# Optimization experiments

Measured on AMD Instinct MI355X. Metric: run time of the kernel, lower is better.

The kernel has to match this reference:

```python
import jax, jax.numpy as jnp
import numpy as np

EMB = 1024
HEADS = 16
B, N = 2, 2048

def setup_inputs() -> dict:
    key = jax.random.key(0)
    ks = jax.random.split(key, 9)
    s = 1.0 / np.sqrt(EMB)
    return {
        "x": jax.random.normal(ks[0], (B, N, EMB), dtype=jnp.float32),
        "Wq": jax.random.normal(ks[1], (EMB, EMB), dtype=jnp.float32) * s,
        "bq": jax.random.normal(ks[2], (EMB,), dtype=jnp.float32) * 0.01,
        "Wk": jax.random.normal(ks[3], (EMB, EMB), dtype=jnp.float32) * s,
        "bk": jax.random.normal(ks[4], (EMB,), dtype=jnp.float32) * 0.01,
        "Wv": jax.random.normal(ks[5], (EMB, EMB), dtype=jnp.float32) * s,
        "bv": jax.random.normal(ks[6], (EMB,), dtype=jnp.float32) * 0.01,
        "Wo": jax.random.normal(ks[7], (EMB, EMB), dtype=jnp.float32) * s,
        "bo": jax.random.normal(ks[8], (EMB,), dtype=jnp.float32) * 0.01,
    }

def _split_heads(t):
    b, n, e = t.shape
    return t.reshape(b, n, HEADS, e // HEADS).transpose(0, 2, 1, 3)  # b h n d

def reference(x, Wq, bq, Wk, bk, Wv, bv, Wo, bo):
    q = _split_heads(x @ Wq + bq)
    k = _split_heads(x @ Wk + bk)
    v = _split_heads(x @ Wv + bv)
    # NOTE: original scales by sqrt(emb_size), not sqrt(head_dim)
    scaling = jnp.asarray(EMB, x.dtype) ** 0.5
    energy = jnp.einsum('bhqd,bhkd->bhqk', q, k)
    att = jax.nn.softmax(energy / scaling, axis=-1)
    out = jnp.einsum('bhqk,bhkd->bhqd', att, v)
    out = out.transpose(0, 2, 1, 3).reshape(x.shape[0], x.shape[1], EMB)
    return out @ Wo + bo
```

## Files before the change

kernel.cpp:

```cpp
#include <hip/hip_runtime.h>
#include <hip/hip_bf16.h>

typedef __bf16 bf16_t;
typedef bf16_t bf16x8 __attribute__((ext_vector_type(8)));
typedef float f32x4 __attribute__((ext_vector_type(4)));
typedef float f32x16 __attribute__((ext_vector_type(16)));

#define EMB 1024
#define HEADS 16
#define BATCH 2
#define SEQ 2048
#define HD 64
#define TOKENS (BATCH * SEQ)

__device__ __forceinline__ void gld16(bf16_t* lds_dst, const bf16_t* g_src) {
    __builtin_amdgcn_global_load_lds(
        (const __attribute__((address_space(1))) unsigned int*)g_src,
        (__attribute__((address_space(3))) unsigned int*)lds_dst, 16, 0, 0);
}

__device__ __forceinline__ unsigned cvt_pk_bf16(float lo, float hi) {
    unsigned r;
    asm("v_cvt_pk_bf16_f32 %0, %1, %2" : "=v"(r) : "v"(lo), "v"(hi));
    return r;
}

__device__ __forceinline__ float exp2_fast(float x) {
#if __has_builtin(__builtin_amdgcn_exp2f)
    return __builtin_amdgcn_exp2f(x);
#else
    return __expf(x * 0.69314718056f);
#endif
}

#define WAITV(N) asm volatile("s_waitcnt vmcnt(" #N ")" ::: "memory")
#define BAR() __builtin_amdgcn_s_barrier()

__global__ __launch_bounds__(256) void convert_x(const float* __restrict__ x,
                                                 bf16_t* __restrict__ xb) {
    size_t i = ((size_t)blockIdx.x * 256 + threadIdx.x) * 16;
    f32x4 v0 = *(const f32x4*)&x[i];
    f32x4 v1 = *(const f32x4*)&x[i + 4];
    f32x4 v2 = *(const f32x4*)&x[i + 8];
    f32x4 v3 = *(const f32x4*)&x[i + 12];
    bf16x8 o0, o1;
#pragma unroll
    for (int j = 0; j < 4; ++j) {
        o0[j] = (bf16_t)v0[j]; o0[4 + j] = (bf16_t)v1[j];
        o1[j] = (bf16_t)v2[j]; o1[4 + j] = (bf16_t)v3[j];
    }
    *(bf16x8*)&xb[i] = o0;
    *(bf16x8*)&xb[i + 8] = o1;
}

__global__ __launch_bounds__(256) void prep_w(
    const float* __restrict__ W0, const float* __restrict__ W1,
    const float* __restrict__ W2, const float* __restrict__ W3,
    bf16_t* __restrict__ T0, bf16_t* __restrict__ T1,
    bf16_t* __restrict__ T2, bf16_t* __restrict__ T3) {
    __shared__ __align__(16) bf16_t T[64][72];
    int z = blockIdx.z;
    const float* src = (z == 0) ? W0 : (z == 1) ? W1 : (z == 2) ? W2 : W3;
    bf16_t* dst = (z == 0) ? T0 : (z == 1) ? T1 : (z == 2) ? T2 : T3;
    int k0 = blockIdx.y * 64, n0 = blockIdx.x * 64;
    int r = threadIdx.x >> 2, c4 = (threadIdx.x & 3) * 16;
    f32x4 v[4];
#pragma unroll
    for (int q = 0; q < 4; ++q)
        v[q] = *(const f32x4*)&src[(size_t)(k0 + r) * 1024 + n0 + c4 + q * 4];
#pragma unroll
    for (int j = 0; j < 16; ++j) T[c4 + j][r] = (bf16_t)v[j >> 2][j & 3];
    __syncthreads();
    bf16x8 o0 = *(const bf16x8*)&T[r][c4];
    bf16x8 o1 = *(const bf16x8*)&T[r][c4 + 8];
    *(bf16x8*)&dst[(size_t)(n0 + r) * 1024 + k0 + c4] = o0;
    *(bf16x8*)&dst[(size_t)(n0 + r) * 1024 + k0 + c4 + 8] = o1;
}

template <typename TO>
__global__ __launch_bounds__(512) void gemm256(
    const bf16_t* __restrict__ A, const bf16_t* __restrict__ W,
    const float* __restrict__ b0, const float* __restrict__ b1, const float* __restrict__ b2,
    TO* __restrict__ o0, TO* __restrict__ o1, TO* __restrict__ o2,
    int md0, int md1, int md2, float sc0, float sc1, float sc2,
    int MP, int CM, int CSH, int NP) {
    __shared__ __align__(16) bf16_t As[3][256 * 64];
    __shared__ __align__(16) bf16_t Bs[3][128 * 64];

    const int tid = threadIdx.x, w = tid >> 6, lane = tid & 63;
    const int quad = lane >> 4, c = lane & 15;
    const int wm = (w >> 1) * 64, wn = (w & 1) * 64;

    const int lin = blockIdx.x;
    const int xc = lin & 7, t = lin >> 3;
    const int mi = MP * (xc & CM) + (t % MP);
    const int ni = NP * (xc >> CSH) + (t / MP);
    const int m0 = mi * 256, n0 = ni * 128;

    const int z = n0 >> 10;
    const float* bias = (z == 0) ? b0 : (z == 1) ? b1 : b2;
    TO* out = (z == 0) ? o0 : (z == 1) ? o1 : o2;
    const int mode = (z == 0) ? md0 : (z == 1) ? md1 : md2;
    const float scale = (z == 0) ? sc0 : (z == 1) ? sc1 : sc2;
    const int nz = n0 & 1023;

    f32x4 acc[4][4];
#pragma unroll
    for (int i = 0; i < 4; ++i)
#pragma unroll
        for (int j = 0; j < 4; ++j) acc[i][j] = (f32x4){0.f, 0.f, 0.f, 0.f};

    const int r8 = lane >> 3, sg = lane & 7;
    const int g8 = (sg ^ r8) * 8;
    const bf16_t* Ag = A + (size_t)m0 * 1024;
    const bf16_t* Bg = W + (size_t)n0 * 1024;
    int gA[4], lA[4], gB[2], lB[2];
#pragma unroll
    for (int s = 0; s < 4; ++s) {
        lA[s] = (w * 32 + s * 8) * 64;
        gA[s] = (w * 32 + s * 8 + r8) * 1024 + g8;
    }
#pragma unroll
    for (int s = 0; s < 2; ++s) {
        lB[s] = (w * 16 + s * 8) * 64;
        gB[s] = (w * 16 + s * 8 + r8) * 1024 + g8;
    }

    const int so = (quad ^ (c & 7)) * 8;
    int rA[4], rB[4];
#pragma unroll
    for (int i = 0; i < 4; ++i) {
        rA[i] = (wm + i * 16 + c) * 64;
        rB[i] = (wn + i * 16 + c) * 64;
    }

#define STAGE(BUF, T)                                                          \
    {                                                                          \
        int kn = (T) * 64;                                                     \
        _Pragma("unroll")                                                      \
        for (int s = 0; s < 4; ++s) gld16(&As[BUF][lA[s]], &Ag[gA[s] + kn]);   \
        _Pragma("unroll")                                                      \
        for (int s = 0; s < 2; ++s) gld16(&Bs[BUF][lB[s]], &Bg[gB[s] + kn]);   \
    }

#define FRAGS(CUR)                                                             \
    {                                                                          \
        _Pragma("unroll")                                                      \
        for (int ks = 0; ks < 2; ++ks) {                                       \
            int sk = so ^ (ks << 5);                                           \
            bf16x8 af[4], bfv[4];                                              \
            _Pragma("unroll")                                                  \
            for (int i = 0; i < 4; ++i)                                        \
                af[i] = *(const bf16x8*)&As[CUR][rA[i] + sk];                  \
            _Pragma("unroll")                                                  \
            for (int i = 0; i < 4; ++i)                                        \
                bfv[i] = *(const bf16x8*)&Bs[CUR][rB[i] + sk];                 \
            __builtin_amdgcn_s_setprio(1);                                     \
            _Pragma("unroll")                                                  \
            for (int mt = 0; mt < 4; ++mt)                                     \
                _Pragma("unroll")                                              \
                for (int nt = 0; nt < 4; ++nt)                                 \
                    acc[mt][nt] = __builtin_amdgcn_mfma_f32_16x16x32_bf16(     \
                        af[mt], bfv[nt], acc[mt][nt], 0, 0, 0);                \
            __builtin_amdgcn_s_setprio(0);                                     \
        }                                                                      \
    }

#define GSTEP(T, CUR)                                                          \
    {                                                                          \
        WAITV(6);                                                              \
        BAR();                                                                 \
        STAGE(((CUR) + 2) % 3, (T) + 2)                                        \
        FRAGS(CUR)                                                             \
    }

    STAGE(0, 0)
    STAGE(1, 1)
    for (int T = 0; T < 12; T += 3) {
        GSTEP(T, 0)
        GSTEP(T + 1, 1)
        GSTEP(T + 2, 2)
    }
    GSTEP(12, 0)
    GSTEP(13, 1)
    WAITV(6); BAR(); FRAGS(2)
    WAITV(0); BAR(); FRAGS(0)
#undef GSTEP
#undef FRAGS
#undef STAGE

    typedef TO TOx4 __attribute__((ext_vector_type(4)));
#pragma unroll
    for (int nt = 0; nt < 4; ++nt) {
        int colz = nz + wn + nt * 16 + c;
        float bv = bias[colz];
#pragma unroll
        for (int mt = 0; mt < 4; ++mt) {
            if (mode == 2) {
                int row = m0 + wm + mt * 16 + quad * 4;
                int bb = row >> 11, n = row & 2047;
                int hh = colz >> 6, d = colz & 63;
                TOx4 pk;
#pragma unroll
                for (int r = 0; r < 4; ++r)
                    pk[r] = (TO)((acc[mt][nt][r] + bv) * scale);
                *(TOx4*)&out[((size_t)(bb * HEADS + hh) * HD + d) * SEQ + n] = pk;
            } else {
#pragma unroll
                for (int r = 0; r < 4; ++r) {
                    int row = m0 + wm + mt * 16 + quad * 4 + r;
                    float v = (acc[mt][nt][r] + bv) * scale;
                    size_t idx;
                    if (mode == 0) {
                        idx = (size_t)row * 1024 + colz;
                    } else {
                        int bb = row >> 11, n = row & 2047;
                        int hh = colz >> 6, d = colz & 63;
                        idx = ((size_t)(bb * HEADS + hh) * SEQ + n) * HD + d;
                    }
                    out[idx] = (TO)v;
                }
            }
        }
    }
}

__global__ __launch_bounds__(256) void attn_kernel(
    const bf16_t* __restrict__ Q, const bf16_t* __restrict__ K,
    const bf16_t* __restrict__ Vt, bf16_t* __restrict__ O) {
    __shared__ __align__(16) bf16_t Qs[128 * 64];
    __shared__ __align__(16) bf16_t Ks[3][64 * 64];
    __shared__ __align__(16) bf16_t Vs[3][64 * 64];

    const int tid = threadIdx.x, w = tid >> 6, lane = tid & 63;
    const int hi = lane >> 5, lq = lane & 31;

    const int lin = blockIdx.x + (blockIdx.y << 4);
    const int xcd = lin & 7, slot = lin >> 3;
    const int bh = xcd + ((slot >> 4) << 3);
    const int q0 = (slot & 15) << 7;
    const int b = bh >> 4, h = bh & 15;

    const int srow8 = lane >> 3, sch = lane & 7;

    const bf16_t* Qg = Q + ((size_t)bh * SEQ + q0) * HD;
    const bf16_t* Kg0 = K + (size_t)bh * SEQ * HD;
    const bf16_t* Vg0 = Vt + (size_t)bh * HD * SEQ;

    int sl[2], sgK[2], sgV[2];
#pragma unroll
    for (int s = 0; s < 2; ++s) {
        int rg = (w * 2 + s) * 8;
        int row = rg + srow8;
        int g = sch ^ (row & 7);
        sl[s] = rg * 64;
        sgK[s] = row * 64 + g * 8;
        sgV[s] = row * SEQ + g * 8;
    }
    int rd[4];
#pragma unroll
    for (int dc = 0; dc < 4; ++dc)
        rd[dc] = lq * 64 + (((dc * 2 + hi) ^ (lq & 7)) * 8);

#pragma unroll
    for (int s = 0; s < 4; ++s) {
        int rg = (w * 4 + s) * 8;
        int row = rg + srow8;
        int g = sch ^ (row & 7);
        gld16(&Qs[rg * 64], &Qg[(size_t)row * 64 + g * 8]);
    }
#pragma unroll
    for (int s = 0; s < 2; ++s) {
        gld16(&Ks[0][sl[s]], &Kg0[sgK[s]]);
        gld16(&Vs[0][sl[s]], &Vg0[sgV[s]]);
    }
#pragma unroll
    for (int s = 0; s < 2; ++s) {
        gld16(&Ks[1][sl[s]], &Kg0[64 * HD + sgK[s]]);
        gld16(&Vs[1][sl[s]], &Vg0[64 + sgV[s]]);
    }

    WAITV(8);
    BAR();
    bf16x8 qf[4];
#pragma unroll
    for (int dc = 0; dc < 4; ++dc)
        qf[dc] = *(const bf16x8*)&Qs[w * 2048 + rd[dc]];

    f32x16 Oacc0, Oacc1;
#pragma unroll
    for (int r = 0; r < 16; ++r) { Oacc0[r] = 0.f; Oacc1[r] = 0.f; }
    float lp = 0.f;

    const bf16_t* KgN = Kg0 + 2 * 64 * HD;
    const bf16_t* VgN = Vg0 + 2 * 64;

#define PACKFRAG(SS, c2, dstIdx)                                               \
        {                                                                      \
            unsigned pa = cvt_pk_bf16(SS[8 * (c2) + 0], SS[8 * (c2) + 1]);     \
            unsigned pb = cvt_pk_bf16(SS[8 * (c2) + 4], SS[8 * (c2) + 5]);     \
            unsigned pc = cvt_pk_bf16(SS[8 * (c2) + 2], SS[8 * (c2) + 3]);     \
            unsigned pd = cvt_pk_bf16(SS[8 * (c2) + 6], SS[8 * (c2) + 7]);     \
            asm volatile("v_permlane32_swap_b32 %0, %1" : "+v"(pa), "+v"(pb)); \
            asm volatile("v_permlane32_swap_b32 %0, %1" : "+v"(pc), "+v"(pd)); \
            union { unsigned u[4]; bf16x8 v; } pu;                             \
            pu.u[0] = pa; pu.u[1] = pc; pu.u[2] = pb; pu.u[3] = pd;            \
            pf[dstIdx] = pu.v;                                                 \
        }

#define ACORE(CUR)                                                             \
    {                                                                          \
        f32x16 St0, St1;                                                       \
        _Pragma("unroll")                                                      \
        for (int r = 0; r < 16; ++r) { St0[r] = 0.f; St1[r] = 0.f; }           \
        __builtin_amdgcn_s_setprio(1);                                         \
        _Pragma("unroll")                                                      \
        for (int dc = 0; dc < 4; ++dc) {                                       \
            bf16x8 k0 = *(const bf16x8*)&Ks[CUR][rd[dc]];                      \
            bf16x8 k1 = *(const bf16x8*)&Ks[CUR][rd[dc] + 2048];               \
            St0 = __builtin_amdgcn_mfma_f32_32x32x16_bf16(k0, qf[dc], St0, 0, 0, 0); \
            St1 = __builtin_amdgcn_mfma_f32_32x32x16_bf16(k1, qf[dc], St1, 0, 0, 0); \
        }                                                                      \
        __builtin_amdgcn_s_setprio(0);                                         \
        _Pragma("unroll")                                                      \
        for (int r = 0; r < 16; ++r) {                                         \
            St0[r] = exp2_fast(St0[r]); lp += St0[r];                          \
            St1[r] = exp2_fast(St1[r]); lp += St1[r];                          \
        }                                                                      \
        bf16x8 pf[4];                                                          \
        PACKFRAG(St0, 0, 0) PACKFRAG(St0, 1, 1)                                \
        PACKFRAG(St1, 0, 2) PACKFRAG(St1, 1, 3)                                \
        __builtin_amdgcn_s_setprio(1);                                         \
        _Pragma("unroll")                                                      \
        for (int f = 0; f < 4; ++f) {                                          \
            bf16x8 v0 = *(const bf16x8*)&Vs[CUR][rd[f]];                       \
            bf16x8 v1 = *(const bf16x8*)&Vs[CUR][rd[f] + 2048];                \
            Oacc0 = __builtin_amdgcn_mfma_f32_32x32x16_bf16(pf[f], v0, Oacc0, 0, 0, 0); \
            Oacc1 = __builtin_amdgcn_mfma_f32_32x32x16_bf16(pf[f], v1, Oacc1, 0, 0, 0); \
        }                                                                      \
        __builtin_amdgcn_s_setprio(0);                                         \
    }

#define ASTEP(CUR)                                                             \
    {                                                                          \
        WAITV(4);                                                              \
        BAR();                                                                 \
        _Pragma("unroll")                                                      \
        for (int s = 0; s < 2; ++s) {                                          \
            gld16(&Ks[((CUR) + 2) % 3][sl[s]], &KgN[sgK[s]]);                  \
            gld16(&Vs[((CUR) + 2) % 3][sl[s]], &VgN[sgV[s]]);                  \
        }                                                                      \
        KgN += 64 * HD; VgN += 64;                                             \
        ACORE(CUR)                                                             \
    }

    for (int t = 0; t < 30; t += 3) {
        ASTEP(0) ASTEP(1) ASTEP(2)
    }
    WAITV(4); BAR(); ACORE(0)
    WAITV(0); BAR(); ACORE(1)
#undef ASTEP
#undef ACORE
#undef PACKFRAG

    lp += __shfl_xor(lp, 32);
    float rl = 1.0f / lp;

#pragma unroll
    for (int r = 0; r < 16; ++r) {
        int q_loc = (r & 3) + 8 * (r >> 2) + 4 * hi;
        float rr = __shfl(rl, q_loc);
        int qrow = q0 + w * 32 + q_loc;
        size_t base = ((size_t)(b * SEQ + qrow)) * EMB + h * 64;
        O[base + lq] = (bf16_t)(Oacc0[r] * rr);
        O[base + 32 + lq] = (bf16_t)(Oacc1[r] * rr);
    }
}

extern "C" void kernel_launch(void* const* d_in, const int* in_sizes, int n_in,
                              void* d_out, int out_size, void* d_ws, size_t ws_size,
                              hipStream_t stream) {
    (void)in_sizes; (void)n_in; (void)out_size; (void)ws_size;
    const float* x  = (const float*)d_in[0];
    const float* Wq = (const float*)d_in[1];
    const float* bq = (const float*)d_in[2];
    const float* Wk = (const float*)d_in[3];
    const float* bk = (const float*)d_in[4];
    const float* Wv = (const float*)d_in[5];
    const float* bv = (const float*)d_in[6];
    const float* Wo = (const float*)d_in[7];
    const float* bo = (const float*)d_in[8];

    bf16_t* ws = (bf16_t*)d_ws;
    const size_t NELEM = (size_t)TOKENS * EMB;
    const size_t WELEM = (size_t)EMB * EMB;
    bf16_t* Qb  = ws;
    bf16_t* Kb  = ws + NELEM;
    bf16_t* Vtb = ws + 2 * NELEM;
    bf16_t* Ob  = ws + 3 * NELEM;
    bf16_t* xb  = ws + 4 * NELEM;
    bf16_t* Wt0 = ws + 5 * NELEM;
    bf16_t* Wt1 = Wt0 + WELEM;
    bf16_t* Wt2 = Wt0 + 2 * WELEM;
    bf16_t* Wt3 = Wt0 + 3 * WELEM;

    hipLaunchKernelGGL(convert_x, dim3(1024), dim3(256), 0, stream, x, xb);
    hipLaunchKernelGGL(prep_w, dim3(16, 16, 4), dim3(256), 0, stream,
                       Wq, Wk, Wv, Wo, Wt0, Wt1, Wt2, Wt3);
    hipLaunchKernelGGL((gemm256<bf16_t>), dim3(384), dim3(512), 0, stream,
                       xb, Wt0, bq, bk, bv, Qb, Kb, Vtb,
                       1, 1, 2, 0.0450842204f, 1.0f, 1.0f,
                       4, 3, 2, 12);
    hipLaunchKernelGGL(attn_kernel, dim3(16, 32), dim3(256), 0, stream, Qb, Kb, Vtb, Ob);
    hipLaunchKernelGGL((gemm256<float>), dim3(128), dim3(512), 0, stream,
                       Ob, Wt3, bo, bo, bo,
                       (float*)d_out, (float*)d_out, (float*)d_out,
                       0, 0, 0, 1.0f, 1.0f, 1.0f,
                       2, 7, 3, 8);
}
```

Before: 203.7 us.

## Merge prep kernels, load Q directly to registers, trim attention inner loop

Fuses the x conversion and weight transpose kernels into one launch, which removes a kernel launch and its tail. In attention, Q fragments are loaded straight from global memory into registers instead of going through LDS, which drops the Q shared buffer and the initial barrier. The first QK MFMA now uses a zero accumulator instead of explicitly zeroing the scores. The softmax row sum is split into paired vector accumulators to shorten the dependency chain. The direct Q loads are uncoalesced 16-byte reads, and the smaller LDS footprint may change occupancy.

```diff
diff --git a/kernel.cpp b/kernel.cpp
--- a/kernel.cpp
+++ b/kernel.cpp
@@ -4,6 +4,7 @@
 typedef __bf16 bf16_t;
 typedef bf16_t bf16x8 __attribute__((ext_vector_type(8)));
 typedef float f32x4 __attribute__((ext_vector_type(4)));
+typedef float f32x2 __attribute__((ext_vector_type(2)));
 typedef float f32x16 __attribute__((ext_vector_type(16)));
 
 #define EMB 1024
@@ -36,33 +37,34 @@
 #define WAITV(N) asm volatile("s_waitcnt vmcnt(" #N ")" ::: "memory")
 #define BAR() __builtin_amdgcn_s_barrier()
 
-__global__ __launch_bounds__(256) void convert_x(const float* __restrict__ x,
-                                                 bf16_t* __restrict__ xb) {
-    size_t i = ((size_t)blockIdx.x * 256 + threadIdx.x) * 16;
-    f32x4 v0 = *(const f32x4*)&x[i];
-    f32x4 v1 = *(const f32x4*)&x[i + 4];
-    f32x4 v2 = *(const f32x4*)&x[i + 8];
-    f32x4 v3 = *(const f32x4*)&x[i + 12];
-    bf16x8 o0, o1;
-#pragma unroll
-    for (int j = 0; j < 4; ++j) {
-        o0[j] = (bf16_t)v0[j]; o0[4 + j] = (bf16_t)v1[j];
-        o1[j] = (bf16_t)v2[j]; o1[4 + j] = (bf16_t)v3[j];
-    }
-    *(bf16x8*)&xb[i] = o0;
-    *(bf16x8*)&xb[i + 8] = o1;
-}
-
-__global__ __launch_bounds__(256) void prep_w(
+__global__ __launch_bounds__(256) void prep_all(
+    const float* __restrict__ x, bf16_t* __restrict__ xb,
     const float* __restrict__ W0, const float* __restrict__ W1,
     const float* __restrict__ W2, const float* __restrict__ W3,
     bf16_t* __restrict__ T0, bf16_t* __restrict__ T1,
     bf16_t* __restrict__ T2, bf16_t* __restrict__ T3) {
     __shared__ __align__(16) bf16_t T[64][72];
-    int z = blockIdx.z;
+    if (blockIdx.x < 1024) {
+        size_t i = ((size_t)blockIdx.x * 256 + threadIdx.x) * 16;
+        f32x4 v0 = *(const f32x4*)&x[i];
+        f32x4 v1 = *(const f32x4*)&x[i + 4];
+        f32x4 v2 = *(const f32x4*)&x[i + 8];
+        f32x4 v3 = *(const f32x4*)&x[i + 12];
+        bf16x8 o0, o1;
+#pragma unroll
+        for (int j = 0; j < 4; ++j) {
+            o0[j] = (bf16_t)v0[j]; o0[4 + j] = (bf16_t)v1[j];
+            o1[j] = (bf16_t)v2[j]; o1[4 + j] = (bf16_t)v3[j];
+        }
+        *(bf16x8*)&xb[i] = o0;
+        *(bf16x8*)&xb[i + 8] = o1;
+        return;
+    }
+    int t = blockIdx.x - 1024;
+    int z = t >> 8, rid = t & 255;
     const float* src = (z == 0) ? W0 : (z == 1) ? W1 : (z == 2) ? W2 : W3;
     bf16_t* dst = (z == 0) ? T0 : (z == 1) ? T1 : (z == 2) ? T2 : T3;
-    int k0 = blockIdx.y * 64, n0 = blockIdx.x * 64;
+    int k0 = (rid >> 4) * 64, n0 = (rid & 15) * 64;
     int r = threadIdx.x >> 2, c4 = (threadIdx.x & 3) * 16;
     f32x4 v[4];
 #pragma unroll
@@ -228,7 +230,6 @@
 __global__ __launch_bounds__(256) void attn_kernel(
     const bf16_t* __restrict__ Q, const bf16_t* __restrict__ K,
     const bf16_t* __restrict__ Vt, bf16_t* __restrict__ O) {
-    __shared__ __align__(16) bf16_t Qs[128 * 64];
     __shared__ __align__(16) bf16_t Ks[3][64 * 64];
     __shared__ __align__(16) bf16_t Vs[3][64 * 64];
 
@@ -243,7 +244,6 @@
 
     const int srow8 = lane >> 3, sch = lane & 7;
 
-    const bf16_t* Qg = Q + ((size_t)bh * SEQ + q0) * HD;
     const bf16_t* Kg0 = K + (size_t)bh * SEQ * HD;
     const bf16_t* Vg0 = Vt + (size_t)bh * HD * SEQ;
 
@@ -262,13 +262,14 @@
     for (int dc = 0; dc < 4; ++dc)
         rd[dc] = lq * 64 + (((dc * 2 + hi) ^ (lq & 7)) * 8);
 
-#pragma unroll
-    for (int s = 0; s < 4; ++s) {
-        int rg = (w * 4 + s) * 8;
-        int row = rg + srow8;
-        int g = sch ^ (row & 7);
-        gld16(&Qs[rg * 64], &Qg[(size_t)row * 64 + g * 8]);
-    }
+    bf16x8 qf[4];
+    {
+        const bf16_t* Qrow = Q + ((size_t)bh * SEQ + q0 + w * 32 + lq) * HD;
+#pragma unroll
+        for (int dc = 0; dc < 4; ++dc)
+            qf[dc] = *(const bf16x8*)&Qrow[(dc * 2 + hi) * 8];
+    }
+
 #pragma unroll
     for (int s = 0; s < 2; ++s) {
         gld16(&Ks[0][sl[s]], &Kg0[sgK[s]]);
@@ -280,17 +281,14 @@
         gld16(&Vs[1][sl[s]], &Vg0[64 + sgV[s]]);
     }
 
-    WAITV(8);
-    BAR();
-    bf16x8 qf[4];
-#pragma unroll
-    for (int dc = 0; dc < 4; ++dc)
-        qf[dc] = *(const bf16x8*)&Qs[w * 2048 + rd[dc]];
+    f32x16 Zf;
+#pragma unroll
+    for (int r = 0; r < 16; ++r) Zf[r] = 0.f;
 
     f32x16 Oacc0, Oacc1;
 #pragma unroll
     for (int r = 0; r < 16; ++r) { Oacc0[r] = 0.f; Oacc1[r] = 0.f; }
-    float lp = 0.f;
+    f32x2 lpA = (f32x2){0.f, 0.f}, lpB = (f32x2){0.f, 0.f};
 
     const bf16_t* KgN = Kg0 + 2 * 64 * HD;
     const bf16_t* VgN = Vg0 + 2 * 64;
@@ -311,11 +309,15 @@
 #define ACORE(CUR)                                                             \
     {                                                                          \
         f32x16 St0, St1;                                                       \
-        _Pragma("unroll")                                                      \
-        for (int r = 0; r < 16; ++r) { St0[r] = 0.f; St1[r] = 0.f; }           \
         __builtin_amdgcn_s_setprio(1);                                         \
-        _Pragma("unroll")                                                      \
-        for (int dc = 0; dc < 4; ++dc) {                                       \
+        {                                                                      \
+            bf16x8 k0 = *(const bf16x8*)&Ks[CUR][rd[0]];                       \
+            bf16x8 k1 = *(const bf16x8*)&Ks[CUR][rd[0] + 2048];                \
+            St0 = __builtin_amdgcn_mfma_f32_32x32x16_bf16(k0, qf[0], Zf, 0, 0, 0); \
+            St1 = __builtin_amdgcn_mfma_f32_32x32x16_bf16(k1, qf[0], Zf, 0, 0, 0); \
+        }                                                                      \
+        _Pragma("unroll")                                                      \
+        for (int dc = 1; dc < 4; ++dc) {                                       \
             bf16x8 k0 = *(const bf16x8*)&Ks[CUR][rd[dc]];                      \
             bf16x8 k1 = *(const bf16x8*)&Ks[CUR][rd[dc] + 2048];               \
             St0 = __builtin_amdgcn_mfma_f32_32x32x16_bf16(k0, qf[dc], St0, 0, 0, 0); \
@@ -323,9 +325,11 @@
         }                                                                      \
         __builtin_amdgcn_s_setprio(0);                                         \
         _Pragma("unroll")                                                      \
-        for (int r = 0; r < 16; ++r) {                                         \
-            St0[r] = exp2_fast(St0[r]); lp += St0[r];                          \
-            St1[r] = exp2_fast(St1[r]); lp += St1[r];                          \
+        for (int r = 0; r < 16; r += 2) {                                      \
+            St0[r] = exp2_fast(St0[r]); St0[r + 1] = exp2_fast(St0[r + 1]);    \
+            lpA += (f32x2){St0[r], St0[r + 1]};                                \
+            St1[r] = exp2_fast(St1[r]); St1[r + 1] = exp2_fast(St1[r + 1]);    \
+            lpB += (f32x2){St1[r], St1[r + 1]};                                \
         }                                                                      \
         bf16x8 pf[4];                                                          \
         PACKFRAG(St0, 0, 0) PACKFRAG(St0, 1, 1)                                \
@@ -363,6 +367,7 @@
 #undef ACORE
 #undef PACKFRAG
 
+    float lp = (lpA[0] + lpA[1]) + (lpB[0] + lpB[1]);
     lp += __shfl_xor(lp, 32);
     float rl = 1.0f / lp;
 
@@ -403,10 +408,10 @@
     bf16_t* Wt1 = Wt0 + WELEM;
     bf16_t* Wt2 = Wt0 + 2 * WELEM;
     bf16_t* Wt3 = Wt0 + 3 * WELEM;
-
-    hipLaunchKernelGGL(convert_x, dim3(1024), dim3(256), 0, stream, x, xb);
-    hipLaunchKernelGGL(prep_w, dim3(16, 16, 4), dim3(256), 0, stream,
-                       Wq, Wk, Wv, Wo, Wt0, Wt1, Wt2, Wt3);
+    (void)Wt1; (void)Wt2;
+
+    hipLaunchKernelGGL(prep_all, dim3(2048), dim3(256), 0, stream,
+                       x, xb, Wq, Wk, Wv, Wo, Wt0, Wt1, Wt2, Wt3);
     hipLaunchKernelGGL((gemm256<bf16_t>), dim3(384), dim3(512), 0, stream,
                        xb, Wt0, bq, bk, bv, Qb, Kb, Vtb,
                        1, 1, 2, 0.0450842204f, 1.0f, 1.0f,
```

Result: no change. 202.7 us (-0.5%).
